# Optimization experiments

Measured on AMD Instinct MI355X. Metric: run time of the kernel, lower is better.

The kernel has to match this reference:

```python
import jax, jax.numpy as jnp
import numpy as np

N, E, D = 20000, 320000, 128
H1, H2, H3 = 256, 512, 1024
SLOPE = 0.01  # LeakyReLU default
EPS = 1e-5    # BatchNorm eps

def _leaky(x):
    return jnp.where(x >= 0, x, SLOPE * x)

def setup_inputs() -> dict:
    key = jax.random.key(0)
    ks = jax.random.split(key, 12)
    def lin(k, fi, fo):
        bound = 1.0 / np.sqrt(fi)
        kw, kb = jax.random.split(k)
        W = jax.random.uniform(kw, (fi, fo), minval=-bound, maxval=bound, dtype=jnp.float32)
        b = jax.random.uniform(kb, (fo,), minval=-bound, maxval=bound, dtype=jnp.float32)
        return W, b
    x0 = jax.random.normal(ks[0], (N, D), dtype=jnp.float32)
    edge_index = jax.random.randint(ks[1], (2, E), 0, N, dtype=jnp.int64)
    edge_attr = jax.random.uniform(ks[2], (E, D), dtype=jnp.float32)
    W1, b1 = lin(ks[3], D, H1)
    W2, b2 = lin(ks[4], H1, H2)
    W3, b3 = lin(ks[5], D + H2, H3)
    W4, b4 = lin(ks[6], H3, D)
    bn_gamma = jnp.ones((D,), jnp.float32)
    bn_beta = jnp.zeros((D,), jnp.float32)
    bn_mean = jnp.zeros((D,), jnp.float32)
    bn_var = jnp.ones((D,), jnp.float32)
    return dict(x0=x0, edge_index=edge_index, edge_attr=edge_attr,
                W1=W1, b1=b1, W2=W2, b2=b2, W3=W3, b3=b3, W4=W4, b4=b4,
                bn_gamma=bn_gamma, bn_beta=bn_beta, bn_mean=bn_mean, bn_var=bn_var)

def reference(x0, edge_index, edge_attr, W1, b1, W2, b2, W3, b3, W4, b4,
              bn_gamma, bn_beta, bn_mean, bn_var):
    src, dst = edge_index[0], edge_index[1]
    # message: mlp1(x_j * edge_attr)  (eval mode: dropout = identity)
    x_j = x0[src]                                 # [E, D]
    m = _leaky(jnp.dot(x_j * edge_attr, W1) + b1)  # [E, H1]
    m = _leaky(jnp.dot(m, W2) + b2)                # [E, H2]
    # aggregate: scatter-add into destination nodes
    aggr = jax.ops.segment_sum(m, dst, num_segments=N)  # [N, H2]
    # update: mlp2(concat) with BN (eval, running stats), residual average
    tmp = jnp.concatenate([x0, aggr], axis=1)           # [N, D+H2]
    h = _leaky(jnp.dot(tmp, W3) + b3)                   # [N, H3]
    h = jnp.dot(h, W4) + b4                             # [N, D]
    h = (h - bn_mean) / jnp.sqrt(bn_var + EPS) * bn_gamma + bn_beta
    return (h + x0) / 2
```

## Files before the change

### kernel.cpp

```cpp
#include <hip/hip_runtime.h>


constexpr int D  = 128;
constexpr int H1 = 256;
constexpr int H2 = 512;
constexpr int H3 = 1024;
constexpr int K3 = D + H2;

typedef short  bf16x8 __attribute__((ext_vector_type(8)));
typedef ushort u16x8  __attribute__((ext_vector_type(8)));
typedef float  f32x4  __attribute__((ext_vector_type(4)));

__device__ __forceinline__ float leaky(float x) { return x >= 0.f ? x : 0.01f * x; }

__device__ __forceinline__ ushort f2bf(float f) {
    unsigned u = __float_as_uint(f);
    u += 0x7FFFu + ((u >> 16) & 1u);
    return (ushort)(u >> 16);
}

__device__ __forceinline__ float bf2f(ushort u) {
    return __uint_as_float(((unsigned)u) << 16);
}

__device__ __forceinline__ int swz(int row, int bytecol) {
    return bytecol ^ ((row & 7) << 4);
}

__device__ __forceinline__ f32x4 mfma16(bf16x8 a, bf16x8 b, f32x4 c) {
    return __builtin_amdgcn_mfma_f32_16x16x32_bf16(a, b, c, 0, 0, 0);
}

__device__ __forceinline__ void gload_lds16(const void* g, void* l) {
    __builtin_amdgcn_global_load_lds(
        (const __attribute__((address_space(1))) void*)g,
        (__attribute__((address_space(3))) void*)l, 16, 0, 0);
}

__global__ __launch_bounds__(256) void hist_kernel(
    const int* __restrict__ dst, int* __restrict__ cursor, int E)
{
    const int i = blockIdx.x * 256 + threadIdx.x;
    if (i < E) atomicAdd(&cursor[dst[i]], 1);
}

__global__ __launch_bounds__(1024) void scan_kernel(
    int* __restrict__ cursor, int* __restrict__ row_start, int n)
{
    __shared__ int sums[1024];
    const int tid  = threadIdx.x;
    const int base = tid * 20;
    int v[20];
    int s = 0;
    #pragma unroll
    for (int i = 0; i < 20; ++i) {
        const int idx = base + i;
        v[i] = (idx < n) ? cursor[idx] : 0;
        s += v[i];
    }
    sums[tid] = s;
    __syncthreads();
    int acc = s;
    for (int d = 1; d < 1024; d <<= 1) {
        const int t = (tid >= d) ? sums[tid - d] : 0;
        __syncthreads();
        acc += t;
        sums[tid] = acc;
        __syncthreads();
    }
    int run = acc - s;
    #pragma unroll
    for (int i = 0; i < 20; ++i) {
        const int idx = base + i;
        if (idx < n) { cursor[idx] = run; row_start[idx] = run; }
        run += v[i];
    }
    if (tid == 1023) row_start[n] = acc;
}

__global__ __launch_bounds__(256) void scatter_kernel(
    const int* __restrict__ src, const int* __restrict__ dst,
    int* __restrict__ cursor, int* __restrict__ se, int* __restrict__ pe,
    int E)
{
    const int i = blockIdx.x * 256 + threadIdx.x;
    if (i < E) {
        const int d   = dst[i];
        const int pos = atomicAdd(&cursor[d], 1);
        se[pos] = src[i];
        pe[pos] = i;
    }
}

__global__ __launch_bounds__(256) void gather_t(
    const float* __restrict__ x0, const float* __restrict__ ea,
    const int* __restrict__ se, const int* __restrict__ pe,
    ushort* __restrict__ t)
{
    const int gid  = blockIdx.x * 256 + threadIdx.x;
    const int e    = gid >> 4;
    const int slot = gid & 15;
    const int s = se[e];
    const int p = pe[e];
    const float4* xp = (const float4*)(x0 + (size_t)s * D + slot * 8);
    const float4* gp = (const float4*)(ea + (size_t)p * D + slot * 8);
    const float4 xa = xp[0], xb = xp[1];
    const float4 ga = gp[0], gb = gp[1];
    u16x8 u;
    u[0] = f2bf(xa.x * ga.x); u[1] = f2bf(xa.y * ga.y);
    u[2] = f2bf(xa.z * ga.z); u[3] = f2bf(xa.w * ga.w);
    u[4] = f2bf(xb.x * gb.x); u[5] = f2bf(xb.y * gb.y);
    u[6] = f2bf(xb.z * gb.z); u[7] = f2bf(xb.w * gb.w);
    const int slot_w = slot ^ (e & 7);
    *(u16x8*)(t + (size_t)e * D + slot_w * 8) = u;
}

__global__ __launch_bounds__(256) void pack_weights(
    const float* __restrict__ W, ushort* __restrict__ Wp, int K, int Nc)
{
    const int KT    = K >> 5;
    const int total = (Nc >> 4) * KT * 64;
    const int idx   = blockIdx.x * 256 + threadIdx.x;
    if (idx >= total) return;
    const int l   = idx & 63;
    const int tt  = idx >> 6;
    const int ks  = tt % KT;
    const int ni  = tt / KT;
    const int col = ni * 16 + (l & 15);
    const int k0  = ks * 32 + (l >> 4) * 8;
    u16x8 u;
    #pragma unroll
    for (int j = 0; j < 8; ++j) u[j] = f2bf(W[(size_t)(k0 + j) * Nc + col]);
    *(u16x8*)(Wp + (size_t)idx * 8) = u;
}

constexpr int TE = 64;

__global__ __launch_bounds__(512) void edge_mlp_dense(
    const ushort* __restrict__ t,
    const ushort* __restrict__ W1p, const float* __restrict__ b1,
    const ushort* __restrict__ W2p, const float* __restrict__ b2,
    ushort* __restrict__ m2)
{
    __shared__ __align__(16) ushort t_lds[TE * D];
    __shared__ __align__(16) ushort m1_lds[TE * H1];
    __shared__ __align__(16) ushort m2_lds[TE * 256];

    const int tid  = threadIdx.x;
    const int e0   = blockIdx.x * TE;
    const int lane = tid & 63;
    const int w    = tid >> 6;
    const int lr   = lane & 15;
    const int lg   = lane >> 4;

    const ushort* gsrc = t + (size_t)e0 * D;
    #pragma unroll
    for (int i = 0; i < 2; ++i) {
        const int c = (w * 2 + i) * 64 + lane;
        gload_lds16(gsrc + (size_t)c * 8, t_lds + (w * 2 + i) * 512);
    }
    __syncthreads();

    {
        f32x4 acc[4][2];
        #pragma unroll
        for (int ntl = 0; ntl < 2; ++ntl) {
            const float b = b1[(w * 2 + ntl) * 16 + lr];
            #pragma unroll
            for (int mt = 0; mt < 4; ++mt) acc[mt][ntl] = (f32x4){b, b, b, b};
        }
        #pragma unroll
        for (int ks = 0; ks < 4; ++ks) {
            bf16x8 af[4];
            #pragma unroll
            for (int mt = 0; mt < 4; ++mt) {
                const int row = mt * 16 + lr;
                af[mt] = *(const bf16x8*)((const char*)t_lds + row * 256 +
                                          swz(row, ks * 64 + lg * 16));
            }
            #pragma unroll
            for (int ntl = 0; ntl < 2; ++ntl) {
                const bf16x8 bf = *(const bf16x8*)(W1p +
                    ((size_t)((w * 2 + ntl) * 4 + ks) * 64 + lane) * 8);
                #pragma unroll
                for (int mt = 0; mt < 4; ++mt)
                    acc[mt][ntl] = mfma16(af[mt], bf, acc[mt][ntl]);
            }
        }
        #pragma unroll
        for (int mt = 0; mt < 4; ++mt)
            #pragma unroll
            for (int ntl = 0; ntl < 2; ++ntl)
                #pragma unroll
                for (int r = 0; r < 4; ++r) {
                    const int row = mt * 16 + lg * 4 + r;
                    const int col = (w * 2 + ntl) * 16 + lr;
                    *(ushort*)((char*)m1_lds + row * 512 + swz(row, col * 2)) =
                        f2bf(leaky(acc[mt][ntl][r]));
                }
    }
    __syncthreads();

    #pragma unroll
    for (int p = 0; p < 2; ++p) {
        f32x4 acc[4][2];
        #pragma unroll
        for (int ntl = 0; ntl < 2; ++ntl) {
            const int nt = p * 16 + w * 2 + ntl;
            const float b = b2[nt * 16 + lr];
            #pragma unroll
            for (int mt = 0; mt < 4; ++mt) acc[mt][ntl] = (f32x4){b, b, b, b};
        }
        #pragma unroll
        for (int ks = 0; ks < 8; ++ks) {
            bf16x8 af[4];
            #pragma unroll
            for (int mt = 0; mt < 4; ++mt) {
                const int row = mt * 16 + lr;
                af[mt] = *(const bf16x8*)((const char*)m1_lds + row * 512 +
                                          swz(row, ks * 64 + lg * 16));
            }
            #pragma unroll
            for (int ntl = 0; ntl < 2; ++ntl) {
                const int nt = p * 16 + w * 2 + ntl;
                const bf16x8 bf = *(const bf16x8*)(W2p +
                    ((size_t)(nt * 8 + ks) * 64 + lane) * 8);
                #pragma unroll
                for (int mt = 0; mt < 4; ++mt)
                    acc[mt][ntl] = mfma16(af[mt], bf, acc[mt][ntl]);
            }
        }
        #pragma unroll
        for (int mt = 0; mt < 4; ++mt)
            #pragma unroll
            for (int ntl = 0; ntl < 2; ++ntl)
                #pragma unroll
                for (int r = 0; r < 4; ++r) {
                    const int row = mt * 16 + lg * 4 + r;
                    const int col = (w * 2 + ntl) * 16 + lr;
                    *(ushort*)((char*)m2_lds + row * 512 + swz(row, col * 2)) =
                        f2bf(leaky(acc[mt][ntl][r]));
                }
        __syncthreads();
        #pragma unroll
        for (int i = 0; i < 4; ++i) {
            const int c    = i * 512 + tid;
            const int row  = c >> 5;
            const int col8 = c & 31;
            const u16x8 v = *(const u16x8*)((const char*)m2_lds + row * 512 +
                                            swz(row, col8 * 16));
            *(u16x8*)(m2 + (size_t)(e0 + row) * H2 + p * 256 + col8 * 8) = v;
        }
        __syncthreads();
    }
}

__global__ __launch_bounds__(512) void aggregate_kernel(
    const ushort* __restrict__ m2, const int* __restrict__ row_start,
    ushort* __restrict__ aggrb)
{
    const int lane = threadIdx.x & 63;
    const int w    = threadIdx.x >> 6;
    const int n    = blockIdx.x * 8 + w;

    const int rs0 = row_start[n], rs1 = row_start[n + 1];
    float acc[8];
    #pragma unroll
    for (int j = 0; j < 8; ++j) acc[j] = 0.f;

    for (int e = rs0; e < rs1; ++e) {
        const u16x8 v = *(const u16x8*)(m2 + (size_t)e * H2 + lane * 8);
        #pragma unroll
        for (int j = 0; j < 8; ++j) acc[j] += bf2f(v[j]);
    }

    u16x8 o;
    #pragma unroll
    for (int j = 0; j < 8; ++j) o[j] = f2bf(acc[j]);
    *(u16x8*)(aggrb + (size_t)n * H2 + lane * 8) = o;
}

constexpr int TN = 32;

__global__ __launch_bounds__(512) void node_mlp1_mfma(
    const float* __restrict__ x0, const ushort* __restrict__ aggrb,
    const ushort* __restrict__ W3p, const float* __restrict__ b3,
    ushort* __restrict__ h)
{
    __shared__ __align__(16) ushort a_lds[TN * K3];
    const int tid  = threadIdx.x;
    const int n0   = blockIdx.x * TN;
    const int ch   = blockIdx.y;
    const int lane = tid & 63;
    const int w    = tid >> 6;
    const int lr   = lane & 15;
    const int lg   = lane >> 4;

    #pragma unroll
    for (int i = 0; i < 5; ++i) {
        const int c    = i * 512 + tid;
        const int row  = c / 80;
        const int slot = c % 80;
        u16x8 u;
        if (slot < 16) {
            const float* sp = x0 + (size_t)(n0 + row) * D + slot * 8;
            const float4 va = ((const float4*)sp)[0];
            const float4 vb = ((const float4*)sp)[1];
            u[0] = f2bf(va.x); u[1] = f2bf(va.y); u[2] = f2bf(va.z); u[3] = f2bf(va.w);
            u[4] = f2bf(vb.x); u[5] = f2bf(vb.y); u[6] = f2bf(vb.z); u[7] = f2bf(vb.w);
        } else {
            u = *(const u16x8*)(aggrb + (size_t)(n0 + row) * H2 + (slot - 16) * 8);
        }
        *(u16x8*)((char*)a_lds + row * 1280 + swz(row, slot * 16)) = u;
    }
    __syncthreads();

    f32x4 acc[2][4];
    #pragma unroll
    for (int ntl = 0; ntl < 4; ++ntl) {
        const int colg = ch * 512 + (w * 4 + ntl) * 16 + lr;
        const float b = b3[colg];
        #pragma unroll
        for (int mt = 0; mt < 2; ++mt) acc[mt][ntl] = (f32x4){b, b, b, b};
    }
    for (int ks = 0; ks < 20; ++ks) {
        bf16x8 af[2];
        #pragma unroll
        for (int mt = 0; mt < 2; ++mt) {
            const int row = mt * 16 + lr;
            af[mt] = *(const bf16x8*)((const char*)a_lds + row * 1280 +
                                      swz(row, ks * 64 + lg * 16));
        }
        #pragma unroll
        for (int ntl = 0; ntl < 4; ++ntl) {
            const int nt = ch * 32 + w * 4 + ntl;
            const bf16x8 bf = *(const bf16x8*)(W3p +
                ((size_t)(nt * 20 + ks) * 64 + lane) * 8);
            #pragma unroll
            for (int mt = 0; mt < 2; ++mt)
                acc[mt][ntl] = mfma16(af[mt], bf, acc[mt][ntl]);
        }
    }
    #pragma unroll
    for (int mt = 0; mt < 2; ++mt)
        #pragma unroll
        for (int ntl = 0; ntl < 4; ++ntl) {
            const int colg = ch * 512 + (w * 4 + ntl) * 16 + lr;
            #pragma unroll
            for (int r = 0; r < 4; ++r) {
                const int row = n0 + mt * 16 + lg * 4 + r;
                h[(size_t)row * H3 + colg] = f2bf(leaky(acc[mt][ntl][r]));
            }
        }
}

__global__ __launch_bounds__(256) void node_mlp2_mfma(
    const ushort* __restrict__ h, const float* __restrict__ x0,
    const ushort* __restrict__ W4p, const float* __restrict__ b4,
    const float* __restrict__ gamma, const float* __restrict__ beta,
    const float* __restrict__ mean, const float* __restrict__ var,
    float* __restrict__ out)
{
    const int tid  = threadIdx.x;
    const int n0   = blockIdx.x * TN;
    const int lane = tid & 63;
    const int w    = tid >> 6;
    const int lr   = lane & 15;
    const int lg   = lane >> 4;

    f32x4 acc[2][2];
    #pragma unroll
    for (int ntl = 0; ntl < 2; ++ntl) {
        const float b = b4[(w * 2 + ntl) * 16 + lr];
        #pragma unroll
        for (int mt = 0; mt < 2; ++mt) acc[mt][ntl] = (f32x4){b, b, b, b};
    }
    for (int ks = 0; ks < 32; ++ks) {
        bf16x8 af[2];
        #pragma unroll
        for (int mt = 0; mt < 2; ++mt)
            af[mt] = *(const bf16x8*)(h + (size_t)(n0 + mt * 16 + lr) * H3 +
                                      ks * 32 + lg * 8);
        #pragma unroll
        for (int ntl = 0; ntl < 2; ++ntl) {
            const bf16x8 bf = *(const bf16x8*)(W4p +
                ((size_t)((w * 2 + ntl) * 32 + ks) * 64 + lane) * 8);
            #pragma unroll
            for (int mt = 0; mt < 2; ++mt)
                acc[mt][ntl] = mfma16(af[mt], bf, acc[mt][ntl]);
        }
    }
    #pragma unroll
    for (int ntl = 0; ntl < 2; ++ntl) {
        const int col = (w * 2 + ntl) * 16 + lr;
        const float sc = gamma[col] * rsqrtf(var[col] + 1e-5f);
        const float bo = beta[col] - mean[col] * sc;
        #pragma unroll
        for (int mt = 0; mt < 2; ++mt)
            #pragma unroll
            for (int r = 0; r < 4; ++r) {
                const int row = n0 + mt * 16 + lg * 4 + r;
                const float v = acc[mt][ntl][r] * sc + bo;
                out[(size_t)row * D + col] =
                    0.5f * (v + x0[(size_t)row * D + col]);
            }
    }
}

extern "C" void kernel_launch(void* const* d_in, const int* in_sizes, int n_in,
                              void* d_out, int out_size, void* d_ws, size_t ws_size,
                              hipStream_t stream)
{
    const float* x0    = (const float*)d_in[0];
    const int*   ei    = (const int*)d_in[1];
    const float* ea    = (const float*)d_in[2];
    const float* W1    = (const float*)d_in[3];
    const float* b1    = (const float*)d_in[4];
    const float* W2    = (const float*)d_in[5];
    const float* b2    = (const float*)d_in[6];
    const float* W3    = (const float*)d_in[7];
    const float* b3    = (const float*)d_in[8];
    const float* W4    = (const float*)d_in[9];
    const float* b4    = (const float*)d_in[10];
    const float* gamma = (const float*)d_in[11];
    const float* beta  = (const float*)d_in[12];
    const float* mean  = (const float*)d_in[13];
    const float* var   = (const float*)d_in[14];
    float* out = (float*)d_out;

    const int N = in_sizes[0] / D;
    const int E = in_sizes[2] / D;
    const int* src = ei;
    const int* dst = ei + E;

    char* ws = (char*)d_ws;
    ushort* aggrb = (ushort*)ws;
    ushort* t     = (ushort*)(ws + (size_t)N * H2 * 2);
    ushort* h     = t;
    ushort* m2    = t + (size_t)E * D;
    char*   p2    = (char*)(m2 + (size_t)E * H2);
    int* cursor    = (int*)p2;
    int* row_start = cursor + N;
    int* se        = row_start + N + 1;
    int* pe        = se + E;
    ushort* W1p = (ushort*)(pe + E);
    ushort* W2p = W1p + (size_t)(D  / 32) * (H1 / 16) * 512;
    ushort* W3p = W2p + (size_t)(H1 / 32) * (H2 / 16) * 512;
    ushort* W4p = W3p + (size_t)(K3 / 32) * (H3 / 16) * 512;

    hipMemsetAsync(cursor, 0, (size_t)N * sizeof(int), stream);

    pack_weights<<<(4096  + 255) / 256, 256, 0, stream>>>(W1, W1p, D,  H1);
    pack_weights<<<(16384 + 255) / 256, 256, 0, stream>>>(W2, W2p, H1, H2);
    pack_weights<<<(81920 + 255) / 256, 256, 0, stream>>>(W3, W3p, K3, H3);
    pack_weights<<<(16384 + 255) / 256, 256, 0, stream>>>(W4, W4p, H3, D);

    hist_kernel<<<(E + 255) / 256, 256, 0, stream>>>(dst, cursor, E);
    scan_kernel<<<1, 1024, 0, stream>>>(cursor, row_start, N);
    scatter_kernel<<<(E + 255) / 256, 256, 0, stream>>>(src, dst, cursor,
                                                        se, pe, E);

    gather_t<<<E / 16, 256, 0, stream>>>(x0, ea, se, pe, t);
    edge_mlp_dense<<<E / TE, 512, 0, stream>>>(t, W1p, b1, W2p, b2, m2);
    aggregate_kernel<<<N / 8, 512, 0, stream>>>(m2, row_start, aggrb);

    dim3 g1(N / TN, 2);
    node_mlp1_mfma<<<g1, 512, 0, stream>>>(x0, aggrb, W3p, b3, h);
    node_mlp2_mfma<<<N / TN, 256, 0, stream>>>(h, x0, W4p, b4, gamma, beta, mean, var, out);
}
```

Before: 488.4 us.

## Fuse segment-sum aggregation into node MLP1 kernel prologue

Drops the separate aggregate kernel and its aggrb buffer. The node MLP1 kernel now sums each node's CSR edge rows of m2 directly into shared memory, then computes all 1024 output columns in two passes instead of splitting them across a second grid dimension. This removes a kernel launch and the write and re-read of the aggregated buffer. In exchange the grid is half the size, the GEMM runs longer per block, and the variable-length gather sits on the block's critical path, which may hurt occupancy and latency hiding.

```diff
diff --git a/kernel.cpp b/kernel.cpp
--- a/kernel.cpp
+++ b/kernel.cpp
@@ -255,103 +255,95 @@
     }
 }
 
-__global__ __launch_bounds__(512) void aggregate_kernel(
-    const ushort* __restrict__ m2, const int* __restrict__ row_start,
-    ushort* __restrict__ aggrb)
-{
-    const int lane = threadIdx.x & 63;
-    const int w    = threadIdx.x >> 6;
-    const int n    = blockIdx.x * 8 + w;
-
-    const int rs0 = row_start[n], rs1 = row_start[n + 1];
-    float acc[8];
-    #pragma unroll
-    for (int j = 0; j < 8; ++j) acc[j] = 0.f;
-
-    for (int e = rs0; e < rs1; ++e) {
-        const u16x8 v = *(const u16x8*)(m2 + (size_t)e * H2 + lane * 8);
-        #pragma unroll
-        for (int j = 0; j < 8; ++j) acc[j] += bf2f(v[j]);
-    }
-
-    u16x8 o;
-    #pragma unroll
-    for (int j = 0; j < 8; ++j) o[j] = f2bf(acc[j]);
-    *(u16x8*)(aggrb + (size_t)n * H2 + lane * 8) = o;
-}
-
 constexpr int TN = 32;
 
-__global__ __launch_bounds__(512) void node_mlp1_mfma(
-    const float* __restrict__ x0, const ushort* __restrict__ aggrb,
+__global__ __launch_bounds__(512) void node_mlp1_fused(
+    const float* __restrict__ x0, const ushort* __restrict__ m2,
+    const int* __restrict__ row_start,
     const ushort* __restrict__ W3p, const float* __restrict__ b3,
     ushort* __restrict__ h)
 {
     __shared__ __align__(16) ushort a_lds[TN * K3];
     const int tid  = threadIdx.x;
     const int n0   = blockIdx.x * TN;
-    const int ch   = blockIdx.y;
     const int lane = tid & 63;
     const int w    = tid >> 6;
     const int lr   = lane & 15;
     const int lg   = lane >> 4;
 
-    #pragma unroll
-    for (int i = 0; i < 5; ++i) {
+    {
+        const int row  = tid >> 4;
+        const int slot = tid & 15;
+        const float* sp = x0 + (size_t)(n0 + row) * D + slot * 8;
+        const float4 va = ((const float4*)sp)[0];
+        const float4 vb = ((const float4*)sp)[1];
+        u16x8 u;
+        u[0] = f2bf(va.x); u[1] = f2bf(va.y); u[2] = f2bf(va.z); u[3] = f2bf(va.w);
+        u[4] = f2bf(vb.x); u[5] = f2bf(vb.y); u[6] = f2bf(vb.z); u[7] = f2bf(vb.w);
+        *(u16x8*)((char*)a_lds + row * 1280 + swz(row, slot * 16)) = u;
+    }
+    #pragma unroll
+    for (int i = 0; i < 4; ++i) {
         const int c    = i * 512 + tid;
-        const int row  = c / 80;
-        const int slot = c % 80;
+        const int row  = c >> 6;
+        const int slot = c & 63;
+        const int rs0 = row_start[n0 + row];
+        const int rs1 = row_start[n0 + row + 1];
+        float acc[8];
+        #pragma unroll
+        for (int j = 0; j < 8; ++j) acc[j] = 0.f;
+        for (int e = rs0; e < rs1; ++e) {
+            const u16x8 v = *(const u16x8*)(m2 + (size_t)e * H2 + slot * 8);
+            #pragma unroll
+            for (int j = 0; j < 8; ++j) acc[j] += bf2f(v[j]);
+        }
         u16x8 u;
-        if (slot < 16) {
-            const float* sp = x0 + (size_t)(n0 + row) * D + slot * 8;
-            const float4 va = ((const float4*)sp)[0];
-            const float4 vb = ((const float4*)sp)[1];
-            u[0] = f2bf(va.x); u[1] = f2bf(va.y); u[2] = f2bf(va.z); u[3] = f2bf(va.w);
-            u[4] = f2bf(vb.x); u[5] = f2bf(vb.y); u[6] = f2bf(vb.z); u[7] = f2bf(vb.w);
-        } else {
-            u = *(const u16x8*)(aggrb + (size_t)(n0 + row) * H2 + (slot - 16) * 8);
-        }
-        *(u16x8*)((char*)a_lds + row * 1280 + swz(row, slot * 16)) = u;
+        #pragma unroll
+        for (int j = 0; j < 8; ++j) u[j] = f2bf(acc[j]);
+        *(u16x8*)((char*)a_lds + row * 1280 + swz(row, (16 + slot) * 16)) = u;
     }
     __syncthreads();
 
-    f32x4 acc[2][4];
-    #pragma unroll
-    for (int ntl = 0; ntl < 4; ++ntl) {
-        const int colg = ch * 512 + (w * 4 + ntl) * 16 + lr;
-        const float b = b3[colg];
-        #pragma unroll
-        for (int mt = 0; mt < 2; ++mt) acc[mt][ntl] = (f32x4){b, b, b, b};
-    }
-    for (int ks = 0; ks < 20; ++ks) {
-        bf16x8 af[2];
-        #pragma unroll
-        for (int mt = 0; mt < 2; ++mt) {
-            const int row = mt * 16 + lr;
-            af[mt] = *(const bf16x8*)((const char*)a_lds + row * 1280 +
-                                      swz(row, ks * 64 + lg * 16));
-        }
+    #pragma unroll
+    for (int g = 0; g < 2; ++g) {
+        f32x4 acc[2][4];
         #pragma unroll
         for (int ntl = 0; ntl < 4; ++ntl) {
-            const int nt = ch * 32 + w * 4 + ntl;
-            const bf16x8 bf = *(const bf16x8*)(W3p +
-                ((size_t)(nt * 20 + ks) * 64 + lane) * 8);
-            #pragma unroll
-            for (int mt = 0; mt < 2; ++mt)
-                acc[mt][ntl] = mfma16(af[mt], bf, acc[mt][ntl]);
-        }
-    }
-    #pragma unroll
-    for (int mt = 0; mt < 2; ++mt)
-        #pragma unroll
-        for (int ntl = 0; ntl < 4; ++ntl) {
-            const int colg = ch * 512 + (w * 4 + ntl) * 16 + lr;
-            #pragma unroll
-            for (int r = 0; r < 4; ++r) {
-                const int row = n0 + mt * 16 + lg * 4 + r;
-                h[(size_t)row * H3 + colg] = f2bf(leaky(acc[mt][ntl][r]));
-            }
-        }
+            const int colg = (w * 8 + g * 4 + ntl) * 16 + lr;
+            const float b = b3[colg];
+            #pragma unroll
+            for (int mt = 0; mt < 2; ++mt) acc[mt][ntl] = (f32x4){b, b, b, b};
+        }
+        for (int ks = 0; ks < 20; ++ks) {
+            bf16x8 af[2];
+            #pragma unroll
+            for (int mt = 0; mt < 2; ++mt) {
+                const int row = mt * 16 + lr;
+                af[mt] = *(const bf16x8*)((const char*)a_lds + row * 1280 +
+                                          swz(row, ks * 64 + lg * 16));
+            }
+            #pragma unroll
+            for (int ntl = 0; ntl < 4; ++ntl) {
+                const int nt = w * 8 + g * 4 + ntl;
+                const bf16x8 bf = *(const bf16x8*)(W3p +
+                    ((size_t)(nt * 20 + ks) * 64 + lane) * 8);
+                #pragma unroll
+                for (int mt = 0; mt < 2; ++mt)
+                    acc[mt][ntl] = mfma16(af[mt], bf, acc[mt][ntl]);
+            }
+        }
+        #pragma unroll
+        for (int mt = 0; mt < 2; ++mt)
+            #pragma unroll
+            for (int ntl = 0; ntl < 4; ++ntl) {
+                const int colg = (w * 8 + g * 4 + ntl) * 16 + lr;
+                #pragma unroll
+                for (int r = 0; r < 4; ++r) {
+                    const int row = n0 + mt * 16 + lg * 4 + r;
+                    h[(size_t)row * H3 + colg] = f2bf(leaky(acc[mt][ntl][r]));
+                }
+            }
+    }
 }
 
 __global__ __launch_bounds__(256) void node_mlp2_mfma(
@@ -434,11 +426,10 @@
     const int* dst = ei + E;
 
     char* ws = (char*)d_ws;
-    ushort* aggrb = (ushort*)ws;
-    ushort* t     = (ushort*)(ws + (size_t)N * H2 * 2);
-    ushort* h     = t;
-    ushort* m2    = t + (size_t)E * D;
-    char*   p2    = (char*)(m2 + (size_t)E * H2);
+    ushort* t  = (ushort*)ws;
+    ushort* h  = t;
+    ushort* m2 = t + (size_t)E * D;
+    char*   p2 = (char*)(m2 + (size_t)E * H2);
     int* cursor    = (int*)p2;
     int* row_start = cursor + N;
     int* se        = row_start + N + 1;
@@ -462,9 +453,7 @@
 
     gather_t<<<E / 16, 256, 0, stream>>>(x0, ea, se, pe, t);
     edge_mlp_dense<<<E / TE, 512, 0, stream>>>(t, W1p, b1, W2p, b2, m2);
-    aggregate_kernel<<<N / 8, 512, 0, stream>>>(m2, row_start, aggrb);
-
-    dim3 g1(N / TN, 2);
-    node_mlp1_mfma<<<g1, 512, 0, stream>>>(x0, aggrb, W3p, b3, h);
+
+    node_mlp1_fused<<<N / TN, 512, 0, stream>>>(x0, m2, row_start, W3p, b3, h);
     node_mlp2_mfma<<<N / TN, 256, 0, stream>>>(h, x0, W4p, b4, gamma, beta, mean, var, out);
 }
```

Measured after the change: 525.0 us. +7.5%, slower.
